# Kernel tuning notes

Hardware: AMD Instinct MI355X
Metric: run time of the kernel (lower is better)

Reference implementation:

```python
import jax, jax.numpy as jnp
import numpy as np

B, S, H, A = 8, 512, 256, 64

def setup_inputs() -> dict:
    key = jax.random.key(0)
    k1, k2, k3, k4, k5 = jax.random.split(key, 5)
    def xavier(k, shape):
        fan_in, fan_out = shape[-1], shape[-2] if len(shape) >= 2 else shape[-1]
        limit = float(np.sqrt(6.0 / (fan_in + fan_out)))
        return jax.random.uniform(k, shape, jnp.float32, -limit, limit)
    return {
        "relation_hidden": jax.random.normal(k1, (B, S, H), jnp.float32),
        "w_ta": xavier(k2, (A, H)),
        "w_ja": xavier(k3, (A, H)),
        "b": xavier(k4, (1, 1, 1, A)),
        "v": xavier(k5, (1, A)),
    }

def reference(relation_hidden, w_ta, w_ja, b, v):
    # ta: (B,S,A) scores for 'target', ja: (B,S,A) for 'joint'
    ta = jnp.einsum('bsh,ah->bsa', relation_hidden, w_ta)
    ja = jnp.einsum('bsh,ah->bsa', relation_hidden, w_ja)
    # broadcast-add to (B,S,S,A), tanh, project to scalar with v
    alpha = jnp.tanh(ta[:, :, None, :] + ja[:, None, :, :] + b)  # (B,S,S,A)
    scores = jnp.einsum('bija,a->bij', alpha, v[0])              # (B,S,S)
    return jax.nn.softmax(scores, axis=2)
```

## Files before the change

### kernel.cpp

```cpp
#include <hip/hip_runtime.h>


#define B_ 8
#define S_ 512
#define H_ 256
#define A_ 64

__global__ __launch_bounds__(256) void rel_stage1(
    const float* __restrict__ rh, const float* __restrict__ wta,
    const float* __restrict__ wja, const float* __restrict__ bias,
    float* __restrict__ ta2e, float* __restrict__ ej) {
  __shared__ float rt[64][65];
  const int t = threadIdx.x;
  const int cb = blockIdx.x & 7;
  const int rb = blockIdx.x >> 3;
  const int row0 = rb << 6;
  const int lane = t & 63;
  const int cg = __builtin_amdgcn_readfirstlane(cb * 16 + ((t >> 6) << 2));
  const float* wbase = (cg < A_) ? (wta + (size_t)cg * H_)
                                 : (wja + (size_t)(cg - A_) * H_);
  const float* w0 = wbase;
  const float* w1 = wbase + H_;
  const float* w2 = wbase + 2 * H_;
  const float* w3 = wbase + 3 * H_;

  const int sr = t >> 4;
  const int sq = t & 15;

  float4 acc = {0.f, 0.f, 0.f, 0.f};
  for (int kt = 0; kt < H_; kt += 64) {
    if (kt) __syncthreads();
#pragma unroll
    for (int i = 0; i < 4; ++i) {
      const int r = sr + (i << 4);
      const float4 x =
          *(const float4*)&rh[(size_t)(row0 + r) * H_ + kt + (sq << 2)];
      rt[(sq << 2) + 0][r] = x.x;
      rt[(sq << 2) + 1][r] = x.y;
      rt[(sq << 2) + 2][r] = x.z;
      rt[(sq << 2) + 3][r] = x.w;
    }
    __syncthreads();
#pragma unroll 16
    for (int k = 0; k < 64; ++k) {
      const float x = rt[k][lane];
      const int kk = kt + k;
      acc.x = __builtin_fmaf(x, w0[kk], acc.x);
      acc.y = __builtin_fmaf(x, w1[kk], acc.y);
      acc.z = __builtin_fmaf(x, w2[kk], acc.z);
      acc.w = __builtin_fmaf(x, w3[kk], acc.w);
    }
  }

  const int row = row0 + lane;
  if (cg < A_) {
    float4 e;
    e.x = __expf(2.f * (acc.x + bias[cg + 0]));
    e.y = __expf(2.f * (acc.y + bias[cg + 1]));
    e.z = __expf(2.f * (acc.z + bias[cg + 2]));
    e.w = __expf(2.f * (acc.w + bias[cg + 3]));
    *(float4*)&ta2e[(size_t)row * A_ + cg] = e;
  } else {
    const int a0 = cg - A_;
    const int bidx = row >> 9;
    const int s = row & (S_ - 1);
    float4 e;
    e.x = __expf(2.f * acc.x);
    e.y = __expf(2.f * acc.y);
    e.z = __expf(2.f * acc.z);
    e.w = __expf(2.f * acc.w);
    *(float4*)&ej[((((size_t)bidx * 16 + (a0 >> 2)) * S_ + s) << 2)] = e;
  }
}

__global__ __launch_bounds__(512) void rel_stage2(
    const float* __restrict__ ta2e, const float* __restrict__ ej,
    const float* __restrict__ v, float* __restrict__ out) {
  __shared__ __align__(16) float tai[4][A_];
  __shared__ __align__(16) float vv[A_];
  __shared__ float red[4][8];
  const int t = threadIdx.x;
  const int row0 = blockIdx.x << 2;
  const int bidx = row0 >> 9;
  if (t < 4 * A_) tai[t >> 6][t & 63] = ta2e[(size_t)row0 * A_ + t];
  else if (t < 4 * A_ + A_) vv[t - 4 * A_] = v[t - 4 * A_];
  __syncthreads();

  float vsum = 0.f;
#pragma unroll
  for (int a = 0; a < A_; a += 4) {
    const float4 x = *(const float4*)&vv[a];
    vsum += x.x + x.y + x.z + x.w;
  }

  float acc0 = 0.f, acc1 = 0.f, acc2 = 0.f, acc3 = 0.f;
  const float* ejb = ej + (((size_t)bidx * 16) * S_ << 2) + (t << 2);
#pragma unroll 4
  for (int g = 0; g < 16; ++g) {
    const float4 E = *(const float4*)(ejb + ((size_t)g * S_ << 2));
    const float4 V = *(const float4*)&vv[g << 2];
    const float4 T0 = *(const float4*)&tai[0][g << 2];
    const float4 T1 = *(const float4*)&tai[1][g << 2];
    const float4 T2 = *(const float4*)&tai[2][g << 2];
    const float4 T3 = *(const float4*)&tai[3][g << 2];
    acc0 += V.x * __builtin_amdgcn_rcpf(__builtin_fmaf(T0.x, E.x, 1.f))
          + V.y * __builtin_amdgcn_rcpf(__builtin_fmaf(T0.y, E.y, 1.f))
          + V.z * __builtin_amdgcn_rcpf(__builtin_fmaf(T0.z, E.z, 1.f))
          + V.w * __builtin_amdgcn_rcpf(__builtin_fmaf(T0.w, E.w, 1.f));
    acc1 += V.x * __builtin_amdgcn_rcpf(__builtin_fmaf(T1.x, E.x, 1.f))
          + V.y * __builtin_amdgcn_rcpf(__builtin_fmaf(T1.y, E.y, 1.f))
          + V.z * __builtin_amdgcn_rcpf(__builtin_fmaf(T1.z, E.z, 1.f))
          + V.w * __builtin_amdgcn_rcpf(__builtin_fmaf(T1.w, E.w, 1.f));
    acc2 += V.x * __builtin_amdgcn_rcpf(__builtin_fmaf(T2.x, E.x, 1.f))
          + V.y * __builtin_amdgcn_rcpf(__builtin_fmaf(T2.y, E.y, 1.f))
          + V.z * __builtin_amdgcn_rcpf(__builtin_fmaf(T2.z, E.z, 1.f))
          + V.w * __builtin_amdgcn_rcpf(__builtin_fmaf(T2.w, E.w, 1.f));
    acc3 += V.x * __builtin_amdgcn_rcpf(__builtin_fmaf(T3.x, E.x, 1.f))
          + V.y * __builtin_amdgcn_rcpf(__builtin_fmaf(T3.y, E.y, 1.f))
          + V.z * __builtin_amdgcn_rcpf(__builtin_fmaf(T3.z, E.z, 1.f))
          + V.w * __builtin_amdgcn_rcpf(__builtin_fmaf(T3.w, E.w, 1.f));
  }
  float sc[4] = {vsum - 2.f * acc0, vsum - 2.f * acc1, vsum - 2.f * acc2,
                 vsum - 2.f * acc3};

  const int lane = t & 63;
  const int wv = t >> 6;
#pragma unroll
  for (int r = 0; r < 4; ++r) {
    float m = sc[r];
#pragma unroll
    for (int off = 32; off; off >>= 1) m = fmaxf(m, __shfl_xor(m, off));
    if (lane == 0) red[r][wv] = m;
  }
  __syncthreads();
  float mx[4];
#pragma unroll
  for (int r = 0; r < 4; ++r) {
    float m = red[r][0];
#pragma unroll
    for (int i = 1; i < 8; ++i) m = fmaxf(m, red[r][i]);
    mx[r] = m;
  }
  __syncthreads();
  float ex[4];
#pragma unroll
  for (int r = 0; r < 4; ++r) {
    ex[r] = __expf(sc[r] - mx[r]);
    float s = ex[r];
#pragma unroll
    for (int off = 32; off; off >>= 1) s += __shfl_xor(s, off);
    if (lane == 0) red[r][wv] = s;
  }
  __syncthreads();
#pragma unroll
  for (int r = 0; r < 4; ++r) {
    float s = 0.f;
#pragma unroll
    for (int i = 0; i < 8; ++i) s += red[r][i];
    out[(size_t)(row0 + r) * S_ + t] = ex[r] * __builtin_amdgcn_rcpf(s);
  }
}

extern "C" void kernel_launch(void* const* d_in, const int* in_sizes, int n_in,
                              void* d_out, int out_size, void* d_ws, size_t ws_size,
                              hipStream_t stream) {
  const float* rh   = (const float*)d_in[0];
  const float* wta  = (const float*)d_in[1];
  const float* wja  = (const float*)d_in[2];
  const float* bias = (const float*)d_in[3];
  const float* v    = (const float*)d_in[4];
  float* out = (float*)d_out;

  float* ta2e = (float*)d_ws;
  float* ej   = ta2e + (size_t)B_ * S_ * A_;

  rel_stage1<<<dim3(512), dim3(256), 0, stream>>>(rh, wta, wja, bias, ta2e, ej);
  rel_stage2<<<dim3((B_ * S_) / 4), dim3(512), 0, stream>>>(ta2e, ej, v, out);
}
```

Baseline: 104.7 us.

## Stage weights in LDS for projection and process eight rows per softmax block

Stage 1 now loads the 16 weight rows each block needs into shared memory once per K-tile and reads them as float4, replacing per-thread scalar global weight loads. The block index order also changes so consecutive blocks share a weight group. Stage 2 doubles the rows per block from 4 to 8, so each loaded E vector is reused across more rows. It also folds the -2 factor into the pre-scaled v. The cost is more registers and accumulators in stage 2, plus half as many blocks, which may reduce occupancy and parallelism.

```diff
diff --git a/kernel.cpp b/kernel.cpp
--- a/kernel.cpp
+++ b/kernel.cpp
@@ -11,21 +11,17 @@
     const float* __restrict__ wja, const float* __restrict__ bias,
     float* __restrict__ ta2e, float* __restrict__ ej) {
   __shared__ float rt[64][65];
+  __shared__ __align__(16) float ws[16][68];
   const int t = threadIdx.x;
-  const int cb = blockIdx.x & 7;
-  const int rb = blockIdx.x >> 3;
+  const int rb = blockIdx.x & 63;
+  const int cb = blockIdx.x >> 6;
   const int row0 = rb << 6;
   const int lane = t & 63;
-  const int cg = __builtin_amdgcn_readfirstlane(cb * 16 + ((t >> 6) << 2));
-  const float* wbase = (cg < A_) ? (wta + (size_t)cg * H_)
-                                 : (wja + (size_t)(cg - A_) * H_);
-  const float* w0 = wbase;
-  const float* w1 = wbase + H_;
-  const float* w2 = wbase + 2 * H_;
-  const float* w3 = wbase + 3 * H_;
-
-  const int sr = t >> 4;
-  const int sq = t & 15;
+  const int cg0 = cb << 4;
+  const int cl = __builtin_amdgcn_readfirstlane((t >> 6) << 2);
+  const float* wsrc = (cg0 < A_) ? (wta + (size_t)cg0 * H_)
+                                 : (wja + (size_t)(cg0 - A_) * H_);
+  const int sr = t >> 4, sq = t & 15;
 
   float4 acc = {0.f, 0.f, 0.f, 0.f};
   for (int kt = 0; kt < H_; kt += 64) {
@@ -40,19 +36,30 @@
       rt[(sq << 2) + 2][r] = x.z;
       rt[(sq << 2) + 3][r] = x.w;
     }
+    {
+      const float4 wx =
+          *(const float4*)&wsrc[(size_t)sr * H_ + kt + (sq << 2)];
+      *(float4*)&ws[sr][sq << 2] = wx;
+    }
     __syncthreads();
-#pragma unroll 16
-    for (int k = 0; k < 64; ++k) {
-      const float x = rt[k][lane];
-      const int kk = kt + k;
-      acc.x = __builtin_fmaf(x, w0[kk], acc.x);
-      acc.y = __builtin_fmaf(x, w1[kk], acc.y);
-      acc.z = __builtin_fmaf(x, w2[kk], acc.z);
-      acc.w = __builtin_fmaf(x, w3[kk], acc.w);
+#pragma unroll 4
+    for (int k4 = 0; k4 < 16; ++k4) {
+      const int k = k4 << 2;
+      const float4 w0 = *(const float4*)&ws[cl + 0][k];
+      const float4 w1 = *(const float4*)&ws[cl + 1][k];
+      const float4 w2 = *(const float4*)&ws[cl + 2][k];
+      const float4 w3 = *(const float4*)&ws[cl + 3][k];
+      const float x0 = rt[k + 0][lane], x1 = rt[k + 1][lane];
+      const float x2 = rt[k + 2][lane], x3 = rt[k + 3][lane];
+      acc.x += x0 * w0.x + x1 * w0.y + x2 * w0.z + x3 * w0.w;
+      acc.y += x0 * w1.x + x1 * w1.y + x2 * w1.z + x3 * w1.w;
+      acc.z += x0 * w2.x + x1 * w2.y + x2 * w2.z + x3 * w2.w;
+      acc.w += x0 * w3.x + x1 * w3.y + x2 * w3.z + x3 * w3.w;
     }
   }
 
   const int row = row0 + lane;
+  const int cg = cg0 + cl;
   if (cg < A_) {
     float4 e;
     e.x = __expf(2.f * (acc.x + bias[cg + 0]));
@@ -76,75 +83,65 @@
 __global__ __launch_bounds__(512) void rel_stage2(
     const float* __restrict__ ta2e, const float* __restrict__ ej,
     const float* __restrict__ v, float* __restrict__ out) {
-  __shared__ __align__(16) float tai[4][A_];
-  __shared__ __align__(16) float vv[A_];
-  __shared__ float red[4][8];
+  __shared__ __align__(16) float tai[8][A_];
+  __shared__ __align__(16) float vm[A_];
+  __shared__ float red[8][8];
   const int t = threadIdx.x;
-  const int row0 = blockIdx.x << 2;
+  const int row0 = blockIdx.x << 3;
   const int bidx = row0 >> 9;
-  if (t < 4 * A_) tai[t >> 6][t & 63] = ta2e[(size_t)row0 * A_ + t];
-  else if (t < 4 * A_ + A_) vv[t - 4 * A_] = v[t - 4 * A_];
+  tai[t >> 6][t & 63] = ta2e[(size_t)row0 * A_ + t];
+  if (t < A_) vm[t] = -2.f * v[t];
   __syncthreads();
 
   float vsum = 0.f;
 #pragma unroll
   for (int a = 0; a < A_; a += 4) {
-    const float4 x = *(const float4*)&vv[a];
+    const float4 x = *(const float4*)&vm[a];
     vsum += x.x + x.y + x.z + x.w;
   }
+  vsum *= -0.5f;
 
-  float acc0 = 0.f, acc1 = 0.f, acc2 = 0.f, acc3 = 0.f;
+  float acc[8] = {0.f, 0.f, 0.f, 0.f, 0.f, 0.f, 0.f, 0.f};
   const float* ejb = ej + (((size_t)bidx * 16) * S_ << 2) + (t << 2);
-#pragma unroll 4
+#pragma unroll 2
   for (int g = 0; g < 16; ++g) {
     const float4 E = *(const float4*)(ejb + ((size_t)g * S_ << 2));
-    const float4 V = *(const float4*)&vv[g << 2];
-    const float4 T0 = *(const float4*)&tai[0][g << 2];
-    const float4 T1 = *(const float4*)&tai[1][g << 2];
-    const float4 T2 = *(const float4*)&tai[2][g << 2];
-    const float4 T3 = *(const float4*)&tai[3][g << 2];
-    acc0 += V.x * __builtin_amdgcn_rcpf(__builtin_fmaf(T0.x, E.x, 1.f))
-          + V.y * __builtin_amdgcn_rcpf(__builtin_fmaf(T0.y, E.y, 1.f))
-          + V.z * __builtin_amdgcn_rcpf(__builtin_fmaf(T0.z, E.z, 1.f))
-          + V.w * __builtin_amdgcn_rcpf(__builtin_fmaf(T0.w, E.w, 1.f));
-    acc1 += V.x * __builtin_amdgcn_rcpf(__builtin_fmaf(T1.x, E.x, 1.f))
-          + V.y * __builtin_amdgcn_rcpf(__builtin_fmaf(T1.y, E.y, 1.f))
-          + V.z * __builtin_amdgcn_rcpf(__builtin_fmaf(T1.z, E.z, 1.f))
-          + V.w * __builtin_amdgcn_rcpf(__builtin_fmaf(T1.w, E.w, 1.f));
-    acc2 += V.x * __builtin_amdgcn_rcpf(__builtin_fmaf(T2.x, E.x, 1.f))
-          + V.y * __builtin_amdgcn_rcpf(__builtin_fmaf(T2.y, E.y, 1.f))
-          + V.z * __builtin_amdgcn_rcpf(__builtin_fmaf(T2.z, E.z, 1.f))
-          + V.w * __builtin_amdgcn_rcpf(__builtin_fmaf(T2.w, E.w, 1.f));
-    acc3 += V.x * __builtin_amdgcn_rcpf(__builtin_fmaf(T3.x, E.x, 1.f))
-          + V.y * __builtin_amdgcn_rcpf(__builtin_fmaf(T3.y, E.y, 1.f))
-          + V.z * __builtin_amdgcn_rcpf(__builtin_fmaf(T3.z, E.z, 1.f))
-          + V.w * __builtin_amdgcn_rcpf(__builtin_fmaf(T3.w, E.w, 1.f));
+    const float4 V = *(const float4*)&vm[g << 2];
+#pragma unroll
+    for (int r = 0; r < 8; ++r) {
+      const float4 T = *(const float4*)&tai[r][g << 2];
+      acc[r] += V.x * __builtin_amdgcn_rcpf(__builtin_fmaf(T.x, E.x, 1.f))
+              + V.y * __builtin_amdgcn_rcpf(__builtin_fmaf(T.y, E.y, 1.f))
+              + V.z * __builtin_amdgcn_rcpf(__builtin_fmaf(T.z, E.z, 1.f))
+              + V.w * __builtin_amdgcn_rcpf(__builtin_fmaf(T.w, E.w, 1.f));
+    }
   }
-  float sc[4] = {vsum - 2.f * acc0, vsum - 2.f * acc1, vsum - 2.f * acc2,
-                 vsum - 2.f * acc3};
+  float sc[8];
+#pragma unroll
+  for (int r = 0; r < 8; ++r) sc[r] = vsum + acc[r];
 
   const int lane = t & 63;
   const int wv = t >> 6;
 #pragma unroll
-  for (int r = 0; r < 4; ++r) {
+  for (int r = 0; r < 8; ++r) {
     float m = sc[r];
 #pragma unroll
     for (int off = 32; off; off >>= 1) m = fmaxf(m, __shfl_xor(m, off));
     if (lane == 0) red[r][wv] = m;
   }
   __syncthreads();
-  float mx[4];
+  float mx[8];
 #pragma unroll
-  for (int r = 0; r < 4; ++r) {
+  for (int r = 0; r < 8; ++r) {
     float m = red[r][0];
 #pragma unroll
     for (int i = 1; i < 8; ++i) m = fmaxf(m, red[r][i]);
     mx[r] = m;
   }
   __syncthreads();
-  float ex[4];
+  float ex[8];
 #pragma unroll
-  for (int r = 0; r < 4; ++r) {
+  for (int r = 0; r < 8; ++r) {
     ex[r] = __expf(sc[r] - mx[r]);
     float s = ex[r];
 #pragma unroll
@@ -153,7 +150,7 @@
   }
   __syncthreads();
 #pragma unroll
-  for (int r = 0; r < 4; ++r) {
+  for (int r = 0; r < 8; ++r) {
     float s = 0.f;
 #pragma unroll
     for (int i = 0; i < 8; ++i) s += red[r][i];
@@ -175,5 +172,5 @@
   float* ej   = ta2e + (size_t)B_ * S_ * A_;
 
   rel_stage1<<<dim3(512), dim3(256), 0, stream>>>(rh, wta, wja, bias, ta2e, ej);
-  rel_stage2<<<dim3((B_ * S_) / 4), dim3(512), 0, stream>>>(ta2e, ej, v, out);
+  rel_stage2<<<dim3((B_ * S_) / 8), dim3(512), 0, stream>>>(ta2e, ej, v, out);
 }
```

Result: faster. 101.6 us (-3.0%).
